# Kernel optimization log

Measured on AMD Instinct MI355X. Metric: run time of the kernel, lower is better.

The kernel has to match this reference:

```python
import jax, jax.numpy as jnp
import numpy as np

# Hyperparameters (match init_kwargs)
COORD_DIM = 3
GRID_MIN = -1.0
GRID_MAX = 1.0
N_LEVELS = 16
N_FEATS = 2
LOG2_T = 19
TABLE_SIZE = 2 ** LOG2_T
BASE_RES = 16
FINEST_RES = 512
BSZ = 1048576

_growth = np.exp((np.log(FINEST_RES) - np.log(BASE_RES)) / (N_LEVELS - 1))
RESOLUTIONS = [int(np.floor(BASE_RES * _growth ** i)) for i in range(N_LEVELS)]

# InstantNGP spatial-hash primes (uint32: low bits of the product/xor are
# identical to the int64 computation, and we only keep LOG2_T low bits).
PRIMES = jnp.asarray(np.array([1, 2654435761, 805459861], dtype=np.uint32))
# (8, 3) binary corner offsets of a unit cube.
OFFSETS = jnp.asarray(
    np.array([[(k >> d) & 1 for d in range(COORD_DIM)] for k in range(2 ** COORD_DIM)],
             dtype=np.uint32))
MASK = jnp.uint32(TABLE_SIZE - 1)


def _embed_level(x, table, resolution):
    """x: (B, 3) coords; table: (T, F) hash table. Returns (B, F)."""
    grid_size = (GRID_MAX - GRID_MIN) / resolution
    rel = (x - GRID_MIN) / grid_size                       # (B, 3)
    idx0 = jnp.clip(jnp.floor(rel), 0, resolution - 1)     # bottom-left vertex index
    w = rel - idx0                                         # (B, 3) interp weights in [0,1]
    vidx = idx0.astype(jnp.uint32)[:, None, :] + OFFSETS[None]   # (B, 8, 3)
    # spatial hash: xor of (index * prime) over dims, masked to table size
    vp = vidx * PRIMES[None, None, :]
    h = (vp[..., 0] ^ vp[..., 1] ^ vp[..., 2]) & MASK      # (B, 8) uint32
    verts = table[h.astype(jnp.int32)]                      # (B, 8, F) gather
    # d-linear interpolation weights per corner
    wts = jnp.prod(jnp.where(OFFSETS[None] == 1, w[:, None, :], 1.0 - w[:, None, :]),
                   axis=-1)                                 # (B, 8)
    return jnp.einsum('bv,bvf->bf', wts, verts)             # (B, F)


def setup_inputs() -> dict:
    k1, k2 = jax.random.split(jax.random.key(0))
    x = jax.random.uniform(k1, (BSZ, COORD_DIM), jnp.float32,
                           minval=GRID_MIN, maxval=GRID_MAX)
    embeddings = jax.random.uniform(k2, (N_LEVELS, TABLE_SIZE, N_FEATS), jnp.float32,
                                    minval=-1e-4, maxval=1e-4)
    return {"x": x, "embeddings": embeddings}


def reference(x, embeddings):
    outs = [_embed_level(x, embeddings[i], RESOLUTIONS[i]) for i in range(N_LEVELS)]
    return jnp.concatenate(outs, axis=-1)  # (B, L*F)
```

## Files before the change

kernel.cpp:

```cpp
#include <hip/hip_runtime.h>
#include <hip/hip_fp16.h>
#include <stdint.h>


#define N_LEVELS   16
#define LOG2_T     19
#define TABLE_SIZE (1u << LOG2_T)
#define HASH_MASK  (TABLE_SIZE - 1u)
#define P1 2654435761u
#define P2 805459861u
#define N_CELL     6
#define N_DENSE    8

__constant__ int   c_res[N_LEVELS]   = {16, 20, 25, 32, 40, 50, 64, 80,
                                        101, 128, 161, 203, 256, 322, 406, 512};
__constant__ float c_scale[N_LEVELS] = {8.0f, 10.0f, 12.5f, 16.0f, 20.0f, 25.0f,
                                        32.0f, 40.0f, 50.5f, 64.0f, 80.5f, 101.5f,
                                        128.0f, 161.0f, 203.0f, 256.0f};

__constant__ uint32_t c_coff[N_CELL] = {0, 4096, 12096, 27721, 60489, 124489};
#define CELL_TOTAL 249489u

__constant__ uint32_t c_poff[2] = {0, 270400};
#define PAIR_TOTAL 795280u

__global__ __launch_bounds__(256) void conv_hash(
    const float2* __restrict__ emb, uint32_t* __restrict__ ht, int total)
{
    int i = blockIdx.x * 256 + threadIdx.x;
    if (i >= total) return;
    float2 v = emb[(size_t)N_DENSE * TABLE_SIZE + i];
    __half2 h = __float22half2_rn(v);
    ht[i] = *(uint32_t*)&h;
}

__global__ __launch_bounds__(256) void conv_cell(
    const float2* __restrict__ emb, uint4* __restrict__ cg)
{
    int l = blockIdx.y;
    uint32_t c = blockIdx.x * 256 + threadIdx.x;
    uint32_t R = (uint32_t)c_res[l];
    if (c >= R * R * R) return;
    uint32_t ix = c % R;
    uint32_t r  = c / R;
    uint32_t iy = r % R;
    uint32_t iz = r / R;

    const float2* __restrict__ tb = emb + (size_t)l * TABLE_SIZE;
    uint32_t a0 = ix,      a1 = ix + 1u;
    uint32_t b0 = iy * P1, b1 = b0 + P1;
    uint32_t d0 = iz * P2, d1 = d0 + P2;

    float2 f0 = tb[(a0 ^ b0 ^ d0) & HASH_MASK];
    float2 f1 = tb[(a1 ^ b0 ^ d0) & HASH_MASK];
    float2 f2 = tb[(a0 ^ b1 ^ d0) & HASH_MASK];
    float2 f3 = tb[(a1 ^ b1 ^ d0) & HASH_MASK];
    float2 f4 = tb[(a0 ^ b0 ^ d1) & HASH_MASK];
    float2 f5 = tb[(a1 ^ b0 ^ d1) & HASH_MASK];
    float2 f6 = tb[(a0 ^ b1 ^ d1) & HASH_MASK];
    float2 f7 = tb[(a1 ^ b1 ^ d1) & HASH_MASK];

    __half2 h0 = __float22half2_rn(f0), h1 = __float22half2_rn(f1);
    __half2 h2 = __float22half2_rn(f2), h3 = __float22half2_rn(f3);
    __half2 h4 = __float22half2_rn(f4), h5 = __float22half2_rn(f5);
    __half2 h6 = __float22half2_rn(f6), h7 = __float22half2_rn(f7);

    uint32_t base = 2u * (c_coff[l] + c);
    cg[base]      = make_uint4(*(uint32_t*)&h0, *(uint32_t*)&h1,
                               *(uint32_t*)&h2, *(uint32_t*)&h3);
    cg[base + 1u] = make_uint4(*(uint32_t*)&h4, *(uint32_t*)&h5,
                               *(uint32_t*)&h6, *(uint32_t*)&h7);
}

__global__ __launch_bounds__(256) void conv_pair(
    const float2* __restrict__ emb, uint2* __restrict__ pp)
{
    int li = blockIdx.y;
    int l  = 6 + li;
    uint32_t e = blockIdx.x * 256 + threadIdx.x;
    uint32_t R = (uint32_t)c_res[l];
    uint32_t S = R + 1u;
    if (e >= R * S * S) return;
    uint32_t ix = e % R;
    uint32_t r  = e / R;
    uint32_t iy = r % S;
    uint32_t iz = r / S;
    const float2* __restrict__ tb = emb + (size_t)l * TABLE_SIZE;
    uint32_t hy = iy * P1, hz = iz * P2;
    uint32_t h0 = (ix        ^ hy ^ hz) & HASH_MASK;
    uint32_t h1 = ((ix + 1u) ^ hy ^ hz) & HASH_MASK;
    __half2 a = __float22half2_rn(tb[h0]);
    __half2 b = __float22half2_rn(tb[h1]);
    pp[c_poff[li] + e] = make_uint2(*(uint32_t*)&a, *(uint32_t*)&b);
}

__global__ __launch_bounds__(256) void conv_x4(
    const float* __restrict__ x, float4* __restrict__ x4, int npts)
{
    int b = blockIdx.x * 256 + threadIdx.x;
    if (b >= npts) return;
    size_t xb = (size_t)b * 3;
    x4[b] = make_float4(x[xb], x[xb + 1], x[xb + 2], 0.0f);
}

template <bool X4>
__device__ __forceinline__ void do_point(
    int l, int b, int npts,
    const float*  __restrict__ x,
    const float4* __restrict__ x4,
    const uint32_t* __restrict__ ht,
    const uint4*    __restrict__ cg,
    const uint2*    __restrict__ pp,
    uint32_t* __restrict__ tmp)
{
    if (b >= npts) return;
    float xx, xy, xz;
    if constexpr (X4) {
        float4 v = x4[b];
        xx = v.x; xy = v.y; xz = v.z;
    } else {
        size_t xb = (size_t)b * 3;
        xx = x[xb]; xy = x[xb + 1]; xz = x[xb + 2];
    }

    float scale = c_scale[l];
    float hiv   = (float)c_res[l] - 1.0f;

    float rx = (xx + 1.0f) * scale;
    float ry = (xy + 1.0f) * scale;
    float rz = (xz + 1.0f) * scale;

    float fx = fminf(fmaxf(floorf(rx), 0.0f), hiv);
    float fy = fminf(fmaxf(floorf(ry), 0.0f), hiv);
    float fz = fminf(fmaxf(floorf(rz), 0.0f), hiv);

    float wx = rx - fx, wy = ry - fy, wz = rz - fz;
    uint32_t ix = (uint32_t)fx, iy = (uint32_t)fy, iz = (uint32_t)fz;

    uint32_t u0, u1, u2, u3, u4, u5, u6, u7;
    if (l < N_CELL) {
        uint32_t R    = (uint32_t)c_res[l];
        uint32_t cidx = (iz * R + iy) * R + ix;
        uint32_t base = 2u * (c_coff[l] + cidx);
        uint4 lo = cg[base];
        uint4 hi = cg[base + 1u];
        u0 = lo.x; u1 = lo.y; u2 = lo.z; u3 = lo.w;
        u4 = hi.x; u5 = hi.y; u6 = hi.z; u7 = hi.w;
    } else if (l < N_DENSE) {
        uint32_t R    = (uint32_t)c_res[l];
        uint32_t S    = R + 1u;
        uint32_t base = c_poff[l - N_CELL] + (iz * S + iy) * R + ix;
        uint32_t RS   = R * S;
        uint2 p0 = pp[base];
        uint2 p1 = pp[base + R];
        uint2 p2 = pp[base + RS];
        uint2 p3 = pp[base + RS + R];
        u0 = p0.x; u1 = p0.y; u2 = p1.x; u3 = p1.y;
        u4 = p2.x; u5 = p2.y; u6 = p3.x; u7 = p3.y;
    } else {
        const uint32_t* __restrict__ tb = ht + (size_t)(l - N_DENSE) * TABLE_SIZE;
        uint32_t a0 = ix,      a1 = ix + 1u;
        uint32_t b0 = iy * P1, b1 = b0 + P1;
        uint32_t c0 = iz * P2, c1 = c0 + P2;
        u0 = tb[(a0 ^ b0 ^ c0) & HASH_MASK];
        u1 = tb[(a1 ^ b0 ^ c0) & HASH_MASK];
        u2 = tb[(a0 ^ b1 ^ c0) & HASH_MASK];
        u3 = tb[(a1 ^ b1 ^ c0) & HASH_MASK];
        u4 = tb[(a0 ^ b0 ^ c1) & HASH_MASK];
        u5 = tb[(a1 ^ b0 ^ c1) & HASH_MASK];
        u6 = tb[(a0 ^ b1 ^ c1) & HASH_MASK];
        u7 = tb[(a1 ^ b1 ^ c1) & HASH_MASK];
    }

    float2 v0 = __half22float2(*(__half2*)&u0);
    float2 v1 = __half22float2(*(__half2*)&u1);
    float2 v2 = __half22float2(*(__half2*)&u2);
    float2 v3 = __half22float2(*(__half2*)&u3);
    float2 v4 = __half22float2(*(__half2*)&u4);
    float2 v5 = __half22float2(*(__half2*)&u5);
    float2 v6 = __half22float2(*(__half2*)&u6);
    float2 v7 = __half22float2(*(__half2*)&u7);

    float ux = 1.0f - wx, uy = 1.0f - wy, uz = 1.0f - wz;
    float w0 = ux * uy * uz, w1 = wx * uy * uz;
    float w2 = ux * wy * uz, w3 = wx * wy * uz;
    float w4 = ux * uy * wz, w5 = wx * uy * wz;
    float w6 = ux * wy * wz, w7 = wx * wy * wz;

    float o0 = w0 * v0.x + w1 * v1.x + w2 * v2.x + w3 * v3.x
             + w4 * v4.x + w5 * v5.x + w6 * v6.x + w7 * v7.x;
    float o1 = w0 * v0.y + w1 * v1.y + w2 * v2.y + w3 * v3.y
             + w4 * v4.y + w5 * v5.y + w6 * v6.y + w7 * v7.y;

    __half2 r = __float22half2_rn(make_float2(o0, o1));
    tmp[(size_t)l * npts + b] = *(uint32_t*)&r;
}

template <bool X4>
__global__ __launch_bounds__(256) void gather_lvl(
    const float*  __restrict__ x,
    const float4* __restrict__ x4,
    const uint32_t* __restrict__ ht,
    const uint4*    __restrict__ cg,
    const uint2*    __restrict__ pp,
    uint32_t* __restrict__ tmp, int npts)
{
    const int l  = blockIdx.y;
    const int bA = blockIdx.x * 512 + threadIdx.x;
    do_point<X4>(l, bA,       npts, x, x4, ht, cg, pp, tmp);
    do_point<X4>(l, bA + 256, npts, x, x4, ht, cg, pp, tmp);
}

__global__ __launch_bounds__(256) void transpose_k(
    const uint32_t* __restrict__ tmp, float4* __restrict__ out4, int npts)
{
    __shared__ uint32_t sm[N_LEVELS][514];

    const int b0 = blockIdx.x * 512;
    const int t  = threadIdx.x;

    if (b0 + 512 <= npts) {
        #pragma unroll
        for (int l = 0; l < N_LEVELS; ++l) {
            uint2 u = *(const uint2*)&tmp[(size_t)l * npts + b0 + 2 * t];
            *(uint2*)&sm[l][2 * t] = u;
        }
        __syncthreads();
        #pragma unroll
        for (int k = 0; k < 16; ++k) {
            int q = k * 256 + t;
            int p = q >> 3;
            int j = q & 7;
            uint32_t a = sm[2 * j][p], b = sm[2 * j + 1][p];
            float2 f0 = __half22float2(*(__half2*)&a);
            float2 f1 = __half22float2(*(__half2*)&b);
            out4[(size_t)(b0 + p) * 8 + j] = make_float4(f0.x, f0.y, f1.x, f1.y);
        }
    } else {
        for (int l = 0; l < N_LEVELS; ++l) {
            for (int s = 0; s < 2; ++s) {
                int b = b0 + 2 * t + s;
                if (b < npts) sm[l][2 * t + s] = tmp[(size_t)l * npts + b];
            }
        }
        __syncthreads();
        for (int k = 0; k < 16; ++k) {
            int q = k * 256 + t;
            int p = q >> 3, j = q & 7;
            if (b0 + p < npts) {
                uint32_t a = sm[2 * j][p], b = sm[2 * j + 1][p];
                float2 f0 = __half22float2(*(__half2*)&a);
                float2 f1 = __half22float2(*(__half2*)&b);
                out4[(size_t)(b0 + p) * 8 + j] = make_float4(f0.x, f0.y, f1.x, f1.y);
            }
        }
    }
}

__global__ __launch_bounds__(256) void hash_embed_direct(
    const float* __restrict__ x, const float* __restrict__ emb,
    float2* __restrict__ out, int npts)
{
    int t = blockIdx.x * 256 + threadIdx.x;
    int l = t & 15, b = t >> 4;
    if (b >= npts) return;
    size_t xb = (size_t)b * 3;
    float scale = c_scale[l], hiv = (float)c_res[l] - 1.0f;
    float rx = (x[xb] + 1.0f) * scale, ry = (x[xb+1] + 1.0f) * scale, rz = (x[xb+2] + 1.0f) * scale;
    float fx = fminf(fmaxf(floorf(rx), 0.0f), hiv);
    float fy = fminf(fmaxf(floorf(ry), 0.0f), hiv);
    float fz = fminf(fmaxf(floorf(rz), 0.0f), hiv);
    float wx = rx - fx, wy = ry - fy, wz = rz - fz;
    uint32_t ix = (uint32_t)fx, iy = (uint32_t)fy, iz = (uint32_t)fz;
    uint32_t a0 = ix, a1 = ix + 1u, b0 = iy * P1, b1 = b0 + P1, c0 = iz * P2, c1 = c0 + P2;
    const float2* tb = (const float2*)emb + (size_t)l * TABLE_SIZE;
    float2 v0 = tb[(a0^b0^c0)&HASH_MASK], v1 = tb[(a1^b0^c0)&HASH_MASK];
    float2 v2 = tb[(a0^b1^c0)&HASH_MASK], v3 = tb[(a1^b1^c0)&HASH_MASK];
    float2 v4 = tb[(a0^b0^c1)&HASH_MASK], v5 = tb[(a1^b0^c1)&HASH_MASK];
    float2 v6 = tb[(a0^b1^c1)&HASH_MASK], v7 = tb[(a1^b1^c1)&HASH_MASK];
    float ux = 1.0f - wx, uy = 1.0f - wy, uz = 1.0f - wz;
    float w0 = ux*uy*uz, w1 = wx*uy*uz, w2 = ux*wy*uz, w3 = wx*wy*uz;
    float w4 = ux*uy*wz, w5 = wx*uy*wz, w6 = ux*wy*wz, w7 = wx*wy*wz;
    float o0 = w0*v0.x+w1*v1.x+w2*v2.x+w3*v3.x+w4*v4.x+w5*v5.x+w6*v6.x+w7*v7.x;
    float o1 = w0*v0.y+w1*v1.y+w2*v2.y+w3*v3.y+w4*v4.y+w5*v5.y+w6*v6.y+w7*v7.y;
    out[(size_t)b * N_LEVELS + l] = make_float2(o0, o1);
}

extern "C" void kernel_launch(void* const* d_in, const int* in_sizes, int n_in,
                              void* d_out, int out_size, void* d_ws, size_t ws_size,
                              hipStream_t stream)
{
    const float*  x   = (const float*)d_in[0];
    const float2* emb = (const float2*)d_in[1];
    int npts = in_sizes[0] / 3;

    size_t tmp_bytes = (size_t)npts * N_LEVELS * 4;
    size_t ht_bytes  = (size_t)N_DENSE * TABLE_SIZE * 4;
    size_t cg_bytes  = (size_t)CELL_TOTAL * 32;
    size_t pp_bytes  = (size_t)PAIR_TOTAL * 8;
    size_t x4_bytes  = (size_t)npts * 16;

    int ht_total = N_DENSE * TABLE_SIZE;
    size_t base_need = tmp_bytes + ht_bytes + cg_bytes + pp_bytes;

    if (ws_size >= base_need + x4_bytes) {
        uint32_t* tmp = (uint32_t*)d_ws;
        uint32_t* ht  = (uint32_t*)((char*)d_ws + tmp_bytes);
        uint4*    cg  = (uint4*)   ((char*)d_ws + tmp_bytes + ht_bytes);
        uint2*    pp  = (uint2*)   ((char*)d_ws + tmp_bytes + ht_bytes + cg_bytes);
        float4*   x4  = (float4*)  ((char*)d_ws + base_need);

        hipLaunchKernelGGL(conv_hash, dim3((ht_total + 255) / 256), dim3(256),
                           0, stream, emb, ht, ht_total);
        hipLaunchKernelGGL(conv_cell, dim3(489, N_CELL), dim3(256),
                           0, stream, emb, cg);
        hipLaunchKernelGGL(conv_pair, dim3(2051, 2), dim3(256),
                           0, stream, emb, pp);
        hipLaunchKernelGGL(conv_x4, dim3((npts + 255) / 256), dim3(256),
                           0, stream, x, x4, npts);
        hipLaunchKernelGGL(HIP_KERNEL_NAME(gather_lvl<true>),
                           dim3((npts + 511) / 512, N_LEVELS), dim3(256),
                           0, stream, x, x4, ht, cg, pp, tmp, npts);
        hipLaunchKernelGGL(transpose_k, dim3((npts + 511) / 512), dim3(256),
                           0, stream, tmp, (float4*)d_out, npts);
    } else if (ws_size >= base_need) {
        uint32_t* tmp = (uint32_t*)d_ws;
        uint32_t* ht  = (uint32_t*)((char*)d_ws + tmp_bytes);
        uint4*    cg  = (uint4*)   ((char*)d_ws + tmp_bytes + ht_bytes);
        uint2*    pp  = (uint2*)   ((char*)d_ws + tmp_bytes + ht_bytes + cg_bytes);

        hipLaunchKernelGGL(conv_hash, dim3((ht_total + 255) / 256), dim3(256),
                           0, stream, emb, ht, ht_total);
        hipLaunchKernelGGL(conv_cell, dim3(489, N_CELL), dim3(256),
                           0, stream, emb, cg);
        hipLaunchKernelGGL(conv_pair, dim3(2051, 2), dim3(256),
                           0, stream, emb, pp);
        hipLaunchKernelGGL(HIP_KERNEL_NAME(gather_lvl<false>),
                           dim3((npts + 511) / 512, N_LEVELS), dim3(256),
                           0, stream, x, (const float4*)nullptr, ht, cg, pp,
                           tmp, npts);
        hipLaunchKernelGGL(transpose_k, dim3((npts + 511) / 512), dim3(256),
                           0, stream, tmp, (float4*)d_out, npts);
    } else {
        int total = npts * N_LEVELS;
        hipLaunchKernelGGL(hash_embed_direct, dim3((total + 255) / 256), dim3(256),
                           0, stream, (const float*)x, (const float*)emb,
                           (float2*)d_out, npts);
    }
}
```

Baseline: 486.0 us.

## Fuse table conversion kernels and merge dense levels into one gather block

Merges the three table-conversion kernels into a single launch, drops the x→float4 repack kernel, and changes the gather grid from 16 level slices to 9. The first slice processes all eight dense/cell/pair levels for a point so its coordinates are loaded once. Constant-memory tables become constexpr so level constants fold at compile time. This cuts launch count and repeated x reads, but the y=0 blocks now do eight levels of work each, which creates load imbalance against the single-level hashed blocks.

```diff
diff --git a/kernel.cpp b/kernel.cpp
--- a/kernel.cpp
+++ b/kernel.cpp
@@ -12,73 +12,71 @@
 #define N_CELL     6
 #define N_DENSE    8
 
-__constant__ int   c_res[N_LEVELS]   = {16, 20, 25, 32, 40, 50, 64, 80,
-                                        101, 128, 161, 203, 256, 322, 406, 512};
-__constant__ float c_scale[N_LEVELS] = {8.0f, 10.0f, 12.5f, 16.0f, 20.0f, 25.0f,
-                                        32.0f, 40.0f, 50.5f, 64.0f, 80.5f, 101.5f,
-                                        128.0f, 161.0f, 203.0f, 256.0f};
-
-__constant__ uint32_t c_coff[N_CELL] = {0, 4096, 12096, 27721, 60489, 124489};
+constexpr int      kRes[N_LEVELS]   = {16, 20, 25, 32, 40, 50, 64, 80,
+                                       101, 128, 161, 203, 256, 322, 406, 512};
+constexpr float    kScale[N_LEVELS] = {8.0f, 10.0f, 12.5f, 16.0f, 20.0f, 25.0f,
+                                       32.0f, 40.0f, 50.5f, 64.0f, 80.5f, 101.5f,
+                                       128.0f, 161.0f, 203.0f, 256.0f};
+constexpr uint32_t kCoff[N_CELL] = {0, 4096, 12096, 27721, 60489, 124489};
 #define CELL_TOTAL 249489u
-
-__constant__ uint32_t c_poff[2] = {0, 270400};
+constexpr uint32_t kPoff[2] = {0, 270400};
 #define PAIR_TOTAL 795280u
 
-__global__ __launch_bounds__(256) void conv_hash(
-    const float2* __restrict__ emb, uint32_t* __restrict__ ht, int total)
-{
-    int i = blockIdx.x * 256 + threadIdx.x;
-    if (i >= total) return;
-    float2 v = emb[(size_t)N_DENSE * TABLE_SIZE + i];
-    __half2 h = __float22half2_rn(v);
-    ht[i] = *(uint32_t*)&h;
-}
-
-__global__ __launch_bounds__(256) void conv_cell(
-    const float2* __restrict__ emb, uint4* __restrict__ cg)
-{
-    int l = blockIdx.y;
-    uint32_t c = blockIdx.x * 256 + threadIdx.x;
-    uint32_t R = (uint32_t)c_res[l];
-    if (c >= R * R * R) return;
-    uint32_t ix = c % R;
-    uint32_t r  = c / R;
-    uint32_t iy = r % R;
-    uint32_t iz = r / R;
-
-    const float2* __restrict__ tb = emb + (size_t)l * TABLE_SIZE;
-    uint32_t a0 = ix,      a1 = ix + 1u;
-    uint32_t b0 = iy * P1, b1 = b0 + P1;
-    uint32_t d0 = iz * P2, d1 = d0 + P2;
-
-    float2 f0 = tb[(a0 ^ b0 ^ d0) & HASH_MASK];
-    float2 f1 = tb[(a1 ^ b0 ^ d0) & HASH_MASK];
-    float2 f2 = tb[(a0 ^ b1 ^ d0) & HASH_MASK];
-    float2 f3 = tb[(a1 ^ b1 ^ d0) & HASH_MASK];
-    float2 f4 = tb[(a0 ^ b0 ^ d1) & HASH_MASK];
-    float2 f5 = tb[(a1 ^ b0 ^ d1) & HASH_MASK];
-    float2 f6 = tb[(a0 ^ b1 ^ d1) & HASH_MASK];
-    float2 f7 = tb[(a1 ^ b1 ^ d1) & HASH_MASK];
-
-    __half2 h0 = __float22half2_rn(f0), h1 = __float22half2_rn(f1);
-    __half2 h2 = __float22half2_rn(f2), h3 = __float22half2_rn(f3);
-    __half2 h4 = __float22half2_rn(f4), h5 = __float22half2_rn(f5);
-    __half2 h6 = __float22half2_rn(f6), h7 = __float22half2_rn(f7);
-
-    uint32_t base = 2u * (c_coff[l] + c);
-    cg[base]      = make_uint4(*(uint32_t*)&h0, *(uint32_t*)&h1,
-                               *(uint32_t*)&h2, *(uint32_t*)&h3);
-    cg[base + 1u] = make_uint4(*(uint32_t*)&h4, *(uint32_t*)&h5,
-                               *(uint32_t*)&h6, *(uint32_t*)&h7);
-}
-
-__global__ __launch_bounds__(256) void conv_pair(
-    const float2* __restrict__ emb, uint2* __restrict__ pp)
-{
-    int li = blockIdx.y;
+#define HASH_BLKS 16384
+#define CELL_BLKS 489
+#define PAIR_BLKS 2051
+#define CONV_GRID (HASH_BLKS + N_CELL * CELL_BLKS + 2 * PAIR_BLKS)
+
+__global__ __launch_bounds__(256) void conv_all(
+    const float2* __restrict__ emb, uint32_t* __restrict__ ht,
+    uint4* __restrict__ cg, uint2* __restrict__ pp)
+{
+    int blk = blockIdx.x;
+    if (blk < HASH_BLKS) {
+        int i = blk * 256 + (int)threadIdx.x;
+        float2 v = emb[(size_t)N_DENSE * TABLE_SIZE + i];
+        __half2 h = __float22half2_rn(v);
+        ht[i] = *(uint32_t*)&h;
+        return;
+    }
+    blk -= HASH_BLKS;
+    if (blk < N_CELL * CELL_BLKS) {
+        int l = blk / CELL_BLKS;
+        uint32_t c = (uint32_t)(blk % CELL_BLKS) * 256u + threadIdx.x;
+        uint32_t R = (uint32_t)kRes[l];
+        if (c >= R * R * R) return;
+        uint32_t ix = c % R;
+        uint32_t r  = c / R;
+        uint32_t iy = r % R;
+        uint32_t iz = r / R;
+        const float2* __restrict__ tb = emb + (size_t)l * TABLE_SIZE;
+        uint32_t a0 = ix,      a1 = ix + 1u;
+        uint32_t b0 = iy * P1, b1 = b0 + P1;
+        uint32_t d0 = iz * P2, d1 = d0 + P2;
+        float2 f0 = tb[(a0 ^ b0 ^ d0) & HASH_MASK];
+        float2 f1 = tb[(a1 ^ b0 ^ d0) & HASH_MASK];
+        float2 f2 = tb[(a0 ^ b1 ^ d0) & HASH_MASK];
+        float2 f3 = tb[(a1 ^ b1 ^ d0) & HASH_MASK];
+        float2 f4 = tb[(a0 ^ b0 ^ d1) & HASH_MASK];
+        float2 f5 = tb[(a1 ^ b0 ^ d1) & HASH_MASK];
+        float2 f6 = tb[(a0 ^ b1 ^ d1) & HASH_MASK];
+        float2 f7 = tb[(a1 ^ b1 ^ d1) & HASH_MASK];
+        __half2 h0 = __float22half2_rn(f0), h1 = __float22half2_rn(f1);
+        __half2 h2 = __float22half2_rn(f2), h3 = __float22half2_rn(f3);
+        __half2 h4 = __float22half2_rn(f4), h5 = __float22half2_rn(f5);
+        __half2 h6 = __float22half2_rn(f6), h7 = __float22half2_rn(f7);
+        uint32_t base = 2u * (kCoff[l] + c);
+        cg[base]      = make_uint4(*(uint32_t*)&h0, *(uint32_t*)&h1,
+                                   *(uint32_t*)&h2, *(uint32_t*)&h3);
+        cg[base + 1u] = make_uint4(*(uint32_t*)&h4, *(uint32_t*)&h5,
+                                   *(uint32_t*)&h6, *(uint32_t*)&h7);
+        return;
+    }
+    blk -= N_CELL * CELL_BLKS;
+    int li = blk / PAIR_BLKS;
     int l  = 6 + li;
-    uint32_t e = blockIdx.x * 256 + threadIdx.x;
-    uint32_t R = (uint32_t)c_res[l];
+    uint32_t e = (uint32_t)(blk % PAIR_BLKS) * 256u + threadIdx.x;
+    uint32_t R = (uint32_t)kRes[l];
     uint32_t S = R + 1u;
     if (e >= R * S * S) return;
     uint32_t ix = e % R;
@@ -91,40 +89,18 @@
     uint32_t h1 = ((ix + 1u) ^ hy ^ hz) & HASH_MASK;
     __half2 a = __float22half2_rn(tb[h0]);
     __half2 b = __float22half2_rn(tb[h1]);
-    pp[c_poff[li] + e] = make_uint2(*(uint32_t*)&a, *(uint32_t*)&b);
-}
-
-__global__ __launch_bounds__(256) void conv_x4(
-    const float* __restrict__ x, float4* __restrict__ x4, int npts)
-{
-    int b = blockIdx.x * 256 + threadIdx.x;
-    if (b >= npts) return;
-    size_t xb = (size_t)b * 3;
-    x4[b] = make_float4(x[xb], x[xb + 1], x[xb + 2], 0.0f);
-}
-
-template <bool X4>
-__device__ __forceinline__ void do_point(
-    int l, int b, int npts,
-    const float*  __restrict__ x,
-    const float4* __restrict__ x4,
+    pp[kPoff[li] + e] = make_uint2(*(uint32_t*)&a, *(uint32_t*)&b);
+}
+
+__device__ __forceinline__ void embed_one(
+    int l, int b, int npts, float xx, float xy, float xz,
     const uint32_t* __restrict__ ht,
     const uint4*    __restrict__ cg,
     const uint2*    __restrict__ pp,
     uint32_t* __restrict__ tmp)
 {
-    if (b >= npts) return;
-    float xx, xy, xz;
-    if constexpr (X4) {
-        float4 v = x4[b];
-        xx = v.x; xy = v.y; xz = v.z;
-    } else {
-        size_t xb = (size_t)b * 3;
-        xx = x[xb]; xy = x[xb + 1]; xz = x[xb + 2];
-    }
-
-    float scale = c_scale[l];
-    float hiv   = (float)c_res[l] - 1.0f;
+    float scale = kScale[l];
+    float hiv   = (float)kRes[l] - 1.0f;
 
     float rx = (xx + 1.0f) * scale;
     float ry = (xy + 1.0f) * scale;
@@ -139,17 +115,17 @@
 
     uint32_t u0, u1, u2, u3, u4, u5, u6, u7;
     if (l < N_CELL) {
-        uint32_t R    = (uint32_t)c_res[l];
+        uint32_t R    = (uint32_t)kRes[l];
         uint32_t cidx = (iz * R + iy) * R + ix;
-        uint32_t base = 2u * (c_coff[l] + cidx);
+        uint32_t base = 2u * (kCoff[l] + cidx);
         uint4 lo = cg[base];
         uint4 hi = cg[base + 1u];
         u0 = lo.x; u1 = lo.y; u2 = lo.z; u3 = lo.w;
         u4 = hi.x; u5 = hi.y; u6 = hi.z; u7 = hi.w;
     } else if (l < N_DENSE) {
-        uint32_t R    = (uint32_t)c_res[l];
+        uint32_t R    = (uint32_t)kRes[l];
         uint32_t S    = R + 1u;
-        uint32_t base = c_poff[l - N_CELL] + (iz * S + iy) * R + ix;
+        uint32_t base = kPoff[l - N_CELL] + (iz * S + iy) * R + ix;
         uint32_t RS   = R * S;
         uint2 p0 = pp[base];
         uint2 p1 = pp[base + R];
@@ -196,19 +172,33 @@
     tmp[(size_t)l * npts + b] = *(uint32_t*)&r;
 }
 
-template <bool X4>
 __global__ __launch_bounds__(256) void gather_lvl(
-    const float*  __restrict__ x,
-    const float4* __restrict__ x4,
+    const float* __restrict__ x,
     const uint32_t* __restrict__ ht,
     const uint4*    __restrict__ cg,
     const uint2*    __restrict__ pp,
     uint32_t* __restrict__ tmp, int npts)
 {
-    const int l  = blockIdx.y;
-    const int bA = blockIdx.x * 512 + threadIdx.x;
-    do_point<X4>(l, bA,       npts, x, x4, ht, cg, pp, tmp);
-    do_point<X4>(l, bA + 256, npts, x, x4, ht, cg, pp, tmp);
+    const int y  = blockIdx.y;
+    const int bA = blockIdx.x * 512 + (int)threadIdx.x;
+    const int bB = bA + 256;
+    const bool vA = bA < npts, vB = bB < npts;
+
+    float ax = 0.f, ay = 0.f, az = 0.f, bx = 0.f, by = 0.f, bz = 0.f;
+    if (vA) { size_t p = (size_t)bA * 3; ax = x[p]; ay = x[p+1]; az = x[p+2]; }
+    if (vB) { size_t p = (size_t)bB * 3; bx = x[p]; by = x[p+1]; bz = x[p+2]; }
+
+    if (y == 0) {
+        #pragma unroll
+        for (int l = 0; l < N_DENSE; ++l) {
+            if (vA) embed_one(l, bA, npts, ax, ay, az, ht, cg, pp, tmp);
+            if (vB) embed_one(l, bB, npts, bx, by, bz, ht, cg, pp, tmp);
+        }
+    } else {
+        const int l = 7 + y;
+        if (vA) embed_one(l, bA, npts, ax, ay, az, ht, cg, pp, tmp);
+        if (vB) embed_one(l, bB, npts, bx, by, bz, ht, cg, pp, tmp);
+    }
 }
 
 __global__ __launch_bounds__(256) void transpose_k(
@@ -265,7 +255,7 @@
     int l = t & 15, b = t >> 4;
     if (b >= npts) return;
     size_t xb = (size_t)b * 3;
-    float scale = c_scale[l], hiv = (float)c_res[l] - 1.0f;
+    float scale = kScale[l], hiv = (float)kRes[l] - 1.0f;
     float rx = (x[xb] + 1.0f) * scale, ry = (x[xb+1] + 1.0f) * scale, rz = (x[xb+2] + 1.0f) * scale;
     float fx = fminf(fmaxf(floorf(rx), 0.0f), hiv);
     float fy = fminf(fmaxf(floorf(ry), 0.0f), hiv);
@@ -298,47 +288,18 @@
     size_t ht_bytes  = (size_t)N_DENSE * TABLE_SIZE * 4;
     size_t cg_bytes  = (size_t)CELL_TOTAL * 32;
     size_t pp_bytes  = (size_t)PAIR_TOTAL * 8;
-    size_t x4_bytes  = (size_t)npts * 16;
-
-    int ht_total = N_DENSE * TABLE_SIZE;
-    size_t base_need = tmp_bytes + ht_bytes + cg_bytes + pp_bytes;
-
-    if (ws_size >= base_need + x4_bytes) {
+    size_t need      = tmp_bytes + ht_bytes + cg_bytes + pp_bytes;
+
+    if (ws_size >= need) {
         uint32_t* tmp = (uint32_t*)d_ws;
         uint32_t* ht  = (uint32_t*)((char*)d_ws + tmp_bytes);
         uint4*    cg  = (uint4*)   ((char*)d_ws + tmp_bytes + ht_bytes);
         uint2*    pp  = (uint2*)   ((char*)d_ws + tmp_bytes + ht_bytes + cg_bytes);
-        float4*   x4  = (float4*)  ((char*)d_ws + base_need);
-
-        hipLaunchKernelGGL(conv_hash, dim3((ht_total + 255) / 256), dim3(256),
-                           0, stream, emb, ht, ht_total);
-        hipLaunchKernelGGL(conv_cell, dim3(489, N_CELL), dim3(256),
-                           0, stream, emb, cg);
-        hipLaunchKernelGGL(conv_pair, dim3(2051, 2), dim3(256),
-                           0, stream, emb, pp);
-        hipLaunchKernelGGL(conv_x4, dim3((npts + 255) / 256), dim3(256),
-                           0, stream, x, x4, npts);
-        hipLaunchKernelGGL(HIP_KERNEL_NAME(gather_lvl<true>),
-                           dim3((npts + 511) / 512, N_LEVELS), dim3(256),
-                           0, stream, x, x4, ht, cg, pp, tmp, npts);
-        hipLaunchKernelGGL(transpose_k, dim3((npts + 511) / 512), dim3(256),
-                           0, stream, tmp, (float4*)d_out, npts);
-    } else if (ws_size >= base_need) {
-        uint32_t* tmp = (uint32_t*)d_ws;
-        uint32_t* ht  = (uint32_t*)((char*)d_ws + tmp_bytes);
-        uint4*    cg  = (uint4*)   ((char*)d_ws + tmp_bytes + ht_bytes);
-        uint2*    pp  = (uint2*)   ((char*)d_ws + tmp_bytes + ht_bytes + cg_bytes);
-
-        hipLaunchKernelGGL(conv_hash, dim3((ht_total + 255) / 256), dim3(256),
-                           0, stream, emb, ht, ht_total);
-        hipLaunchKernelGGL(conv_cell, dim3(489, N_CELL), dim3(256),
-                           0, stream, emb, cg);
-        hipLaunchKernelGGL(conv_pair, dim3(2051, 2), dim3(256),
-                           0, stream, emb, pp);
-        hipLaunchKernelGGL(HIP_KERNEL_NAME(gather_lvl<false>),
-                           dim3((npts + 511) / 512, N_LEVELS), dim3(256),
-                           0, stream, x, (const float4*)nullptr, ht, cg, pp,
-                           tmp, npts);
+
+        hipLaunchKernelGGL(conv_all, dim3(CONV_GRID), dim3(256),
+                           0, stream, emb, ht, cg, pp);
+        hipLaunchKernelGGL(gather_lvl, dim3((npts + 511) / 512, 9), dim3(256),
+                           0, stream, x, ht, cg, pp, tmp, npts);
         hipLaunchKernelGGL(transpose_k, dim3((npts + 511) / 512), dim3(256),
                            0, stream, tmp, (float4*)d_out, npts);
     } else {
```

New measurement: 464.9 us. 1.05x faster.
